# Performance work log

Measured on AMD Instinct MI355X. Metric: run time of the kernel, lower is better.

Reference implementation:

```python
import jax, jax.numpy as jnp
import numpy as np
import math

EMBED_DIM = 1024
NUM_HEADS = 16
HEAD_DIM = EMBED_DIM // NUM_HEADS
SEQ = 1024
BATCH = 8


def setup_inputs() -> dict:
    key = jax.random.key(0)
    k1, k2, k3, k4, k5 = jax.random.split(key, 5)
    q = jax.random.normal(k1, (SEQ, BATCH, EMBED_DIM), dtype=jnp.float32)
    # module asserts key == query (self-attention only)
    in_proj_w = jax.random.normal(k2, (3 * EMBED_DIM, EMBED_DIM), dtype=jnp.float32) * 0.02
    in_proj_b = jax.random.normal(k3, (3 * EMBED_DIM,), dtype=jnp.float32) * 0.02
    out_proj_w = jax.random.normal(k4, (EMBED_DIM, EMBED_DIM), dtype=jnp.float32) * 0.02
    out_proj_b = jax.random.normal(k5, (EMBED_DIM,), dtype=jnp.float32) * 0.02
    return {
        "query": q,
        "key": q,
        "value": q,
        "in_proj_w": in_proj_w,
        "in_proj_b": in_proj_b,
        "out_proj_w": out_proj_w,
        "out_proj_b": out_proj_b,
    }


def reference(query, key, value, in_proj_w, in_proj_b, out_proj_w, out_proj_b):
    s, b, e = query.shape
    nh, hd = NUM_HEADS, HEAD_DIM
    norm = math.sqrt(hd)
    # fused QKV projection: [s, b, 3e]
    mixed = query @ in_proj_w.T + in_proj_b
    mixed = mixed.reshape(s, b, nh, 3 * hd)
    q, k, v = jnp.split(mixed, 3, axis=-1)  # each [s, b, nh, hd]
    # -> [b*nh, s, hd]
    q = q.reshape(s, b * nh, hd).transpose(1, 0, 2) / norm
    k = k.reshape(s, b * nh, hd).transpose(1, 0, 2)
    v = v.reshape(s, b * nh, hd).transpose(1, 0, 2)
    # full O(s^2) attention matrix, as in the original bmm/softmax/bmm
    scores = jnp.einsum('nqd,nkd->nqk', q, k)  # [b*nh, s, s]
    probs = jax.nn.softmax(scores, axis=-1)
    ctx = jnp.einsum('nqk,nkd->nqd', probs, v)  # [b*nh, s, hd]
    # [b*nh, s, hd] -> [s, b, e]
    ctx = ctx.reshape(b, nh, s, hd).transpose(2, 0, 1, 3).reshape(s, b, e)
    return ctx @ out_proj_w.T + out_proj_b
```

## Files before the change

### kernel.cpp

```cpp
#include <hip/hip_runtime.h>

typedef __bf16 bf16_t;
typedef __bf16 bf16x4 __attribute__((ext_vector_type(4)));
typedef __bf16 bf16x8 __attribute__((ext_vector_type(8)));
typedef float f32x4 __attribute__((ext_vector_type(4)));

#define MFMA16(a, b, c) __builtin_amdgcn_mfma_f32_16x16x32_bf16((a), (b), (c), 0, 0, 0)

__device__ __forceinline__ const bf16_t* tile_ptr(const bf16_t* t, int row, int kchunk) {
    return t + row * 64 + (((kchunk ^ (row & 7))) << 3);
}

__device__ __forceinline__ void stage64(const bf16_t* __restrict__ gbase, size_t gstride,
                                        bf16_t* lds_rowbase, int lane) {
    const int rr = lane >> 3, cl = lane & 7;
    const bf16_t* g = gbase + (size_t)rr * gstride + ((cl ^ rr) << 3);
    __builtin_amdgcn_global_load_lds((__attribute__((address_space(1))) const void*)g,
                                     (__attribute__((address_space(3))) void*)lds_rowbase,
                                     16, 0, 0);
}

__global__ void __launch_bounds__(256) k_cvt(
    const float* __restrict__ q, const float* __restrict__ wi, const float* __restrict__ wo,
    bf16_t* __restrict__ qb, bf16_t* __restrict__ wib, bf16_t* __restrict__ wob)
{
    const int g = blockIdx.x * 256 + threadIdx.x;
    const float* src; bf16_t* dst; int off;
    if (g < 1048576)      { src = q;  dst = qb;  off = g; }
    else if (g < 1441792) { src = wi; dst = wib; off = g - 1048576; }
    else                  { src = wo; dst = wob; off = g - 1441792; }
    const float4* s4 = (const float4*)(src + (size_t)off * 8);
    float4 a = s4[0], b = s4[1];
    bf16x8 v;
    v[0] = (bf16_t)a.x; v[1] = (bf16_t)a.y; v[2] = (bf16_t)a.z; v[3] = (bf16_t)a.w;
    v[4] = (bf16_t)b.x; v[5] = (bf16_t)b.y; v[6] = (bf16_t)b.z; v[7] = (bf16_t)b.w;
    *(bf16x8*)(dst + (size_t)off * 8) = v;
}

__global__ void __launch_bounds__(512, 2) k_qkv(
    const bf16_t* __restrict__ A, const bf16_t* __restrict__ W,
    const float* __restrict__ bias,
    bf16_t* __restrict__ Qh, bf16_t* __restrict__ Kh, bf16_t* __restrict__ Vt)
{
    __shared__ bf16_t smem[65536];
    bf16_t* const As0 = smem;
    bf16_t* const Bs0 = smem + 16384;
    bf16_t* const As1 = smem + 32768;
    bf16_t* const Bs1 = smem + 49152;

    const int bid = blockIdx.x;
    const int swz = (bid & 7) * 48 + (bid >> 3);
    const int mblk = swz / 12, nblk = swz - mblk * 12;
    const int m0 = mblk * 256;
    const int n0 = nblk * 256;
    const int which = n0 >> 10;
    const int hb0 = (n0 & 1023) >> 6;
    const int t = threadIdx.x;
    const int wid = t >> 6, lane = t & 63;
    const int quad = lane >> 4, l16 = lane & 15;
    const int wm = (wid >> 2) * 128, wn = (wid & 3) * 64;

    f32x4 acc[8][4] = {};

    auto stA = [&](bf16_t* dst, int kt, int p) {
        const int rb = wid * 32 + p * 8;
        stage64(A + (size_t)(m0 + rb) * 1024 + kt * 64, 1024, dst + rb * 64, lane);
    };
    auto stB = [&](bf16_t* dst, int kt, int p) {
        const int rb = wid * 32 + p * 8;
        const int np = n0 + rb;
        const int wrow = ((np & 1023) >> 6) * 192 + which * 64 + (np & 63);
        stage64(W + (size_t)wrow * 1024 + kt * 64, 1024, dst + rb * 64, lane);
    };

#define FENCE()    asm volatile("" ::: "memory")
#define BAR()      do { FENCE(); __builtin_amdgcn_s_barrier(); FENCE(); } while (0)
#define WAIT_LDS() asm volatile("s_waitcnt lgkmcnt(0)" ::: "memory")
#define WAIT_VM()  asm volatile("s_waitcnt vmcnt(0)" ::: "memory")

    auto ktile = [&](const bf16_t* Ac, const bf16_t* Bc, bf16_t* SA, bf16_t* SB,
                     int skt, bool do_st) {
        bf16x8 af[8], b0, b1;
#define LOAD_AF(KS) { _Pragma("unroll") for (int i = 0; i < 8; ++i) \
            af[i] = *(const bf16x8*)tile_ptr(Ac, wm + i * 16 + l16, (KS) * 4 + quad); }
#define LOAD_B(J0, KS) { \
            b0 = *(const bf16x8*)tile_ptr(Bc, wn + (J0) * 16 + l16, (KS) * 4 + quad); \
            b1 = *(const bf16x8*)tile_ptr(Bc, wn + (J0) * 16 + 16 + l16, (KS) * 4 + quad); }
#define MM16(J0) { __builtin_amdgcn_s_setprio(1); \
            _Pragma("unroll") for (int i = 0; i < 8; ++i) { \
                acc[i][J0] = MFMA16(af[i], b0, acc[i][J0]); \
                acc[i][(J0) + 1] = MFMA16(af[i], b1, acc[i][(J0) + 1]); } \
            __builtin_amdgcn_s_setprio(0); }

        if (do_st) { stA(SA, skt, 0); stB(SB, skt, 0); stA(SA, skt, 1); stB(SB, skt, 1); }
        LOAD_AF(0); LOAD_B(0, 0);
        BAR(); WAIT_LDS(); MM16(0); BAR();
        if (do_st) { stA(SA, skt, 2); stB(SB, skt, 2); stA(SA, skt, 3); stB(SB, skt, 3); }
        LOAD_B(2, 0);
        BAR(); WAIT_LDS(); MM16(2); BAR();
        LOAD_AF(1); LOAD_B(0, 1);
        BAR(); WAIT_LDS(); MM16(0); BAR();
        LOAD_B(2, 1);
        BAR(); WAIT_LDS(); MM16(2);
#undef LOAD_AF
#undef LOAD_B
#undef MM16
    };

    #pragma unroll
    for (int p = 0; p < 4; ++p) { stA(As0, 0, p); stB(Bs0, 0, p); }
    WAIT_VM(); BAR();

    #pragma unroll 1
    for (int it = 0; it < 8; ++it) {
        ktile(As0, Bs0, As1, Bs1, 2 * it + 1, true);
        WAIT_VM(); BAR();
        ktile(As1, Bs1, As0, Bs0, 2 * it + 2, it < 7);
        WAIT_VM(); BAR();
    }

    const float scalev = (which == 0) ? 0.180336880111112f : 1.0f;
    #pragma unroll
    for (int j = 0; j < 4; ++j) {
        const int nl = wn + j * 16 + l16;
        const float bv = bias[(hb0 + (nl >> 6)) * 192 + which * 64 + (nl & 63)];
        #pragma unroll
        for (int i = 0; i < 8; ++i) {
            #pragma unroll
            for (int rg = 0; rg < 4; ++rg) {
                const int ml = wm + i * 16 + quad * 4 + rg;
                smem[ml * 256 + (((nl >> 3) ^ ((ml >> 3) & 7)) << 3) + (nl & 7)] =
                    (bf16_t)((acc[i][j][rg] + bv) * scalev);
            }
        }
    }
    __syncthreads();

    const int si0 = m0 >> 3;
    if (which < 2) {
        bf16_t* dst = which ? Kh : Qh;
        #pragma unroll
        for (int u = 0; u < 4; ++u) {
            const int unit = wid * 4 + u;
            const int h = unit >> 3, bi = unit & 7;
            const int head = bi * 16 + hb0 + h;
            #pragma unroll
            for (int pass = 0; pass < 4; ++pass) {
                const int si = pass * 8 + (lane >> 3);
                const int dc = lane & 7;
                const int ml = si * 8 + bi;
                const int nch = (h * 8 + dc) ^ (si & 7);
                bf16x8 v = *(const bf16x8*)&smem[ml * 256 + nch * 8];
                *(bf16x8*)(dst + (size_t)head * 65536 + (size_t)(si0 + si) * 64 + dc * 8) = v;
            }
        }
    } else {
        #pragma unroll
        for (int u = 0; u < 16; ++u) {
            const int unit = wid * 16 + u;
            const int h = unit >> 5, bi = (unit >> 2) & 7, c = unit & 3;
            const int head = bi * 16 + hb0 + h;
            const int d = lane;
            bf16x8 v;
            #pragma unroll
            for (int e = 0; e < 8; ++e) {
                const int ml = (c * 8 + e) * 8 + bi;
                const int nch = (h * 8 + (d >> 3)) ^ e;
                v[e] = smem[ml * 256 + nch * 8 + (d & 7)];
            }
            *(bf16x8*)(Vt + (size_t)head * 65536 +
                       (size_t)(si0 / 8 + c) * 512 + (size_t)d * 8) = v;
        }
    }
#undef FENCE
#undef BAR
#undef WAIT_LDS
#undef WAIT_VM
}

__global__ void __launch_bounds__(256, 4) k_attn(
    const bf16_t* __restrict__ Qh, const bf16_t* __restrict__ Kh,
    const bf16_t* __restrict__ Vg, bf16_t* __restrict__ Ctx)
{
    __shared__ bf16_t Ks[64 * 64];
    __shared__ bf16_t Vts[64 * 64];
    __shared__ bf16_t Pw[4][32 * 64];

    const int bid = blockIdx.x;
    const int head = (bid & 7) * 16 + ((bid >> 3) & 15);
    const int qt = bid >> 7;
    const int t = threadIdx.x;
    const int wave = t >> 6, lane = t & 63;
    const int quad = lane >> 4, l16 = lane & 15;

    const bf16_t* Qg = Qh + (size_t)head * 65536 + (size_t)qt * 8192;
    const bf16_t* Kg = Kh + (size_t)head * 65536;
    const bf16_t* Vgh = Vg + (size_t)head * 65536;

    bf16x8 qf[2][2];
    #pragma unroll
    for (int half = 0; half < 2; ++half)
        #pragma unroll
        for (int ks = 0; ks < 2; ++ks)
            qf[half][ks] = *(const bf16x8*)(
                Qg + (size_t)(wave * 32 + half * 16 + l16) * 64 + ks * 32 + quad * 8);

    bf16x8 ones;
    #pragma unroll
    for (int e = 0; e < 8; ++e) ones[e] = (bf16_t)((l16 == 0) ? 1.0f : 0.0f);

    f32x4 vacc[2][5] = {};

    for (int kt = 0; kt < 16; ++kt) {
        __syncthreads();
        #pragma unroll
        for (int p = 0; p < 2; ++p) {
            const int rb = wave * 16 + p * 8;
            stage64(Kg + (size_t)(kt * 64 + rb) * 64, 64, Ks + rb * 64, lane);
            {
                const int rr = lane >> 3, cl = lane & 7;
                const bf16_t* g = Vgh + (size_t)(kt * 8 + (cl ^ rr)) * 512
                                      + (size_t)(rb + rr) * 8;
                __builtin_amdgcn_global_load_lds(
                    (__attribute__((address_space(1))) const void*)g,
                    (__attribute__((address_space(3))) void*)(Vts + rb * 64), 16, 0, 0);
            }
        }
        __syncthreads();

        f32x4 s[2][4] = {};
        #pragma unroll
        for (int ks = 0; ks < 2; ++ks) {
            #pragma unroll
            for (int j = 0; j < 4; ++j) {
                bf16x8 kf = *(const bf16x8*)tile_ptr(Ks, j * 16 + l16, ks * 4 + quad);
                s[0][j] = MFMA16(kf, qf[0][ks], s[0][j]);
                s[1][j] = MFMA16(kf, qf[1][ks], s[1][j]);
            }
        }

        #pragma unroll
        for (int half = 0; half < 2; ++half) {
            const int row = half * 16 + l16;
            #pragma unroll
            for (int j = 0; j < 4; ++j) {
                bf16x4 pv;
                #pragma unroll
                for (int rg = 0; rg < 4; ++rg)
                    pv[rg] = (bf16_t)exp2f(s[half][j][rg]);
                const int chunk = j * 2 + (quad >> 1);
                *(bf16x4*)&Pw[wave][row * 64 + ((chunk ^ (row & 7)) << 3) + (quad & 1) * 4] = pv;
            }
        }
        asm volatile("s_waitcnt lgkmcnt(0)" ::: "memory");

        #pragma unroll
        for (int ks = 0; ks < 2; ++ks) {
            bf16x8 pf0 = *(const bf16x8*)tile_ptr(Pw[wave], l16, ks * 4 + quad);
            bf16x8 pf1 = *(const bf16x8*)tile_ptr(Pw[wave], 16 + l16, ks * 4 + quad);
            #pragma unroll
            for (int n = 0; n < 4; ++n) {
                bf16x8 vf = *(const bf16x8*)tile_ptr(Vts, n * 16 + l16, ks * 4 + quad);
                vacc[0][n] = MFMA16(pf0, vf, vacc[0][n]);
                vacc[1][n] = MFMA16(pf1, vf, vacc[1][n]);
            }
            vacc[0][4] = MFMA16(pf0, ones, vacc[0][4]);
            vacc[1][4] = MFMA16(pf1, ones, vacc[1][4]);
        }
    }

    const int bi = head >> 4, h = head & 15;
    #pragma unroll
    for (int half = 0; half < 2; ++half) {
        #pragma unroll
        for (int rg = 0; rg < 4; ++rg) {
            const float l = __shfl(vacc[half][4][rg], lane & 48, 64);
            const float inv = 1.0f / l;
            const int si = qt * 128 + wave * 32 + half * 16 + quad * 4 + rg;
            #pragma unroll
            for (int n = 0; n < 4; ++n)
                Ctx[((size_t)si * 8 + bi) * 1024 + h * 64 + n * 16 + l16] =
                    (bf16_t)(vacc[half][n][rg] * inv);
        }
    }
}

__global__ void __launch_bounds__(256) k_out(
    const bf16_t* __restrict__ A, const bf16_t* __restrict__ W,
    const float* __restrict__ bias, float* __restrict__ out)
{
    __shared__ bf16_t As[128 * 64];
    __shared__ bf16_t Bs[128 * 64];
    const int m0 = blockIdx.x * 128;
    const int n0 = blockIdx.y * 128;
    const int t = threadIdx.x;
    const int wave = t >> 6, lane = t & 63;
    const int quad = lane >> 4, l16 = lane & 15;
    const int wm = (wave & 1) * 64, wn = (wave >> 1) * 64;

    f32x4 acc[4][4] = {};

    for (int k0 = 0; k0 < 1024; k0 += 64) {
        __syncthreads();
        #pragma unroll
        for (int p = 0; p < 4; ++p) {
            const int rb = wave * 32 + p * 8;
            stage64(A + (size_t)(m0 + rb) * 1024 + k0, 1024, As + rb * 64, lane);
            stage64(W + (size_t)(n0 + rb) * 1024 + k0, 1024, Bs + rb * 64, lane);
        }
        __syncthreads();
        #pragma unroll
        for (int ks = 0; ks < 2; ++ks) {
            bf16x8 af[4], bf[4];
            #pragma unroll
            for (int i = 0; i < 4; ++i)
                af[i] = *(const bf16x8*)tile_ptr(As, wm + i * 16 + l16, ks * 4 + quad);
            #pragma unroll
            for (int j = 0; j < 4; ++j)
                bf[j] = *(const bf16x8*)tile_ptr(Bs, wn + j * 16 + l16, ks * 4 + quad);
            #pragma unroll
            for (int i = 0; i < 4; ++i)
                #pragma unroll
                for (int j = 0; j < 4; ++j)
                    acc[i][j] = MFMA16(af[i], bf[j], acc[i][j]);
        }
    }

    #pragma unroll
    for (int j = 0; j < 4; ++j) {
        const int n = n0 + wn + j * 16 + l16;
        const float bv = bias[n];
        #pragma unroll
        for (int i = 0; i < 4; ++i) {
            #pragma unroll
            for (int rg = 0; rg < 4; ++rg) {
                const int m = m0 + wm + i * 16 + quad * 4 + rg;
                out[(size_t)m * 1024 + n] = acc[i][j][rg] + bv;
            }
        }
    }
}

extern "C" void kernel_launch(void* const* d_in, const int* in_sizes, int n_in,
                              void* d_out, int out_size, void* d_ws, size_t ws_size,
                              hipStream_t stream)
{
    const float* query = (const float*)d_in[0];
    const float* in_w  = (const float*)d_in[3];
    const float* in_b  = (const float*)d_in[4];
    const float* out_w = (const float*)d_in[5];
    const float* out_b = (const float*)d_in[6];
    float* out = (float*)d_out;

    bf16_t* Wi  = (bf16_t*)d_ws;
    bf16_t* Wo  = Wi + (size_t)3145728;
    bf16_t* Qh  = Wo + (size_t)1048576;
    bf16_t* Kh  = Qh + (size_t)8388608;
    bf16_t* Vt  = Kh + (size_t)8388608;
    bf16_t* Aq  = Vt + (size_t)8388608;
    bf16_t* Ctx = Aq;

    k_cvt<<<dim3(6144), 256, 0, stream>>>(query, in_w, out_w, Aq, Wi, Wo);
    k_qkv<<<dim3(384), 512, 0, stream>>>(Aq, Wi, in_b, Qh, Kh, Vt);
    k_attn<<<dim3(1024), 256, 0, stream>>>(Qh, Kh, Vt, Ctx);
    k_out<<<dim3(64, 8), 256, 0, stream>>>(Ctx, Wo, out_b, out);
}
```

Measured before the change: 286.6 us.

## Deepen QKV GEMM prefetch with partial vmcnt waits across k-tiles

Restructures the QKV projection GEMM's double-buffered main loop. Half of tile t+2 is now loaded into the current buffer right after its compute finishes, while the other half of tile t+1 is issued early. Waits use vmcnt(4) instead of vmcnt(0), so global-to-LDS loads stay in flight across k-tile boundaries and less time is spent stalled on memory. The buffer and wait-count bookkeeping is more intricate, and an off-by-one in staging would be a race risk.

```diff
diff --git a/kernel.cpp b/kernel.cpp
--- a/kernel.cpp
+++ b/kernel.cpp
@@ -76,47 +76,51 @@
 #define FENCE()    asm volatile("" ::: "memory")
 #define BAR()      do { FENCE(); __builtin_amdgcn_s_barrier(); FENCE(); } while (0)
 #define WAIT_LDS() asm volatile("s_waitcnt lgkmcnt(0)" ::: "memory")
-#define WAIT_VM()  asm volatile("s_waitcnt vmcnt(0)" ::: "memory")
-
-    auto ktile = [&](const bf16_t* Ac, const bf16_t* Bc, bf16_t* SA, bf16_t* SB,
-                     int skt, bool do_st) {
+#define WAIT_VM4() asm volatile("s_waitcnt vmcnt(4)" ::: "memory")
+#define WAIT_VM0() asm volatile("s_waitcnt vmcnt(0)" ::: "memory")
+
+#define LOAD_AF(BUF, KS) { _Pragma("unroll") for (int i = 0; i < 8; ++i) \
+        af[i] = *(const bf16x8*)tile_ptr((BUF), wm + i * 16 + l16, (KS) * 4 + quad); }
+#define LOAD_B(BUF, J0, KS) { \
+        b0 = *(const bf16x8*)tile_ptr((BUF), wn + (J0) * 16 + l16, (KS) * 4 + quad); \
+        b1 = *(const bf16x8*)tile_ptr((BUF), wn + (J0) * 16 + 16 + l16, (KS) * 4 + quad); }
+#define MM16(J0) { __builtin_amdgcn_s_setprio(1); \
+        _Pragma("unroll") for (int i = 0; i < 8; ++i) { \
+            acc[i][J0] = MFMA16(af[i], b0, acc[i][J0]); \
+            acc[i][(J0) + 1] = MFMA16(af[i], b1, acc[i][(J0) + 1]); } \
+        __builtin_amdgcn_s_setprio(0); }
+
+    auto ktile = [&](bf16_t* CA, bf16_t* CB, bf16_t* OA, bf16_t* OB, int tt) {
         bf16x8 af[8], b0, b1;
-#define LOAD_AF(KS) { _Pragma("unroll") for (int i = 0; i < 8; ++i) \
-            af[i] = *(const bf16x8*)tile_ptr(Ac, wm + i * 16 + l16, (KS) * 4 + quad); }
-#define LOAD_B(J0, KS) { \
-            b0 = *(const bf16x8*)tile_ptr(Bc, wn + (J0) * 16 + l16, (KS) * 4 + quad); \
-            b1 = *(const bf16x8*)tile_ptr(Bc, wn + (J0) * 16 + 16 + l16, (KS) * 4 + quad); }
-#define MM16(J0) { __builtin_amdgcn_s_setprio(1); \
-            _Pragma("unroll") for (int i = 0; i < 8; ++i) { \
-                acc[i][J0] = MFMA16(af[i], b0, acc[i][J0]); \
-                acc[i][(J0) + 1] = MFMA16(af[i], b1, acc[i][(J0) + 1]); } \
-            __builtin_amdgcn_s_setprio(0); }
-
-        if (do_st) { stA(SA, skt, 0); stB(SB, skt, 0); stA(SA, skt, 1); stB(SB, skt, 1); }
-        LOAD_AF(0); LOAD_B(0, 0);
+        LOAD_AF(CA, 0); LOAD_B(CB, 0, 0);
+        if (tt < 15) { stA(OA, tt + 1, 2); stB(OB, tt + 1, 2);
+                       stA(OA, tt + 1, 3); stB(OB, tt + 1, 3); }
         BAR(); WAIT_LDS(); MM16(0); BAR();
-        if (do_st) { stA(SA, skt, 2); stB(SB, skt, 2); stA(SA, skt, 3); stB(SB, skt, 3); }
-        LOAD_B(2, 0);
+        LOAD_B(CB, 2, 0);
         BAR(); WAIT_LDS(); MM16(2); BAR();
-        LOAD_AF(1); LOAD_B(0, 1);
+        LOAD_AF(CA, 1); LOAD_B(CB, 0, 1);
         BAR(); WAIT_LDS(); MM16(0); BAR();
-        LOAD_B(2, 1);
-        BAR(); WAIT_LDS(); MM16(2);
-#undef LOAD_AF
-#undef LOAD_B
-#undef MM16
+        LOAD_B(CB, 2, 1);
+        BAR(); WAIT_LDS(); MM16(2); BAR();
+        if (tt < 14) {
+            stA(CA, tt + 2, 0); stB(CB, tt + 2, 0);
+            stA(CA, tt + 2, 1); stB(CB, tt + 2, 1);
+            WAIT_VM4();
+        } else {
+            WAIT_VM0();
+        }
+        BAR();
     };
 
     #pragma unroll
     for (int p = 0; p < 4; ++p) { stA(As0, 0, p); stB(Bs0, 0, p); }
-    WAIT_VM(); BAR();
+    stA(As1, 1, 0); stB(Bs1, 1, 0); stA(As1, 1, 1); stB(Bs1, 1, 1);
+    WAIT_VM4(); BAR();
 
     #pragma unroll 1
     for (int it = 0; it < 8; ++it) {
-        ktile(As0, Bs0, As1, Bs1, 2 * it + 1, true);
-        WAIT_VM(); BAR();
-        ktile(As1, Bs1, As0, Bs0, 2 * it + 2, it < 7);
-        WAIT_VM(); BAR();
+        ktile(As0, Bs0, As1, Bs1, 2 * it);
+        ktile(As1, Bs1, As0, Bs0, 2 * it + 1);
     }
 
     const float scalev = (which == 0) ? 0.180336880111112f : 1.0f;
@@ -175,7 +179,11 @@
 #undef FENCE
 #undef BAR
 #undef WAIT_LDS
-#undef WAIT_VM
+#undef WAIT_VM4
+#undef WAIT_VM0
+#undef LOAD_AF
+#undef LOAD_B
+#undef MM16
 }
 
 __global__ void __launch_bounds__(256, 4) k_attn(
```

New measurement: 370.6 us. 29.3% more time.
